# Kernel optimization log

Measured on AMD Instinct MI355X. Metric: run time of the kernel, lower is better.

## Reference

```python
import jax, jax.numpy as jnp
import numpy as np
import math

N_HEAD = 16
N_KV_HEAD = 4
HEAD_DIM = 128  # n_embed // n_head


def apply_rope(x, omega, offset=0):
    # x: (B, T, H, D); omega: (D//2,) Llama-style inverse frequencies
    T = x.shape[1]
    d2 = x.shape[-1] // 2
    pos = (jnp.arange(T) + offset).astype(x.dtype)
    ang = pos[:, None] * omega[None, :]              # (T, d2)
    cos = jnp.cos(ang)[None, :, None, :]
    sin = jnp.sin(ang)[None, :, None, :]
    x1, x2 = x[..., :d2], x[..., d2:]
    return jnp.concatenate([x1 * cos - x2 * sin, x1 * sin + x2 * cos], axis=-1)


def setup_inputs() -> dict:
    key = jax.random.key(0)
    k1, k2, k3, k4 = jax.random.split(key, 4)
    B, T, C = 2, 2048, 2048
    std = 0.02
    x = jax.random.normal(k1, (B, T, C), dtype=jnp.float32)
    wq = jax.random.normal(k2, (C, C), dtype=jnp.float32) * std
    wkv = jax.random.normal(k3, (C, 2 * N_KV_HEAD * HEAD_DIM), dtype=jnp.float32) * std
    wproj = jax.random.normal(k4, (C, C), dtype=jnp.float32) * std * (2 * 24) ** (-0.5)
    # Llama RoPE frequencies: 1 / 10000^(2i/D)
    omega = (1.0 / (10000.0 ** (jnp.arange(0, HEAD_DIM, 2, dtype=jnp.float32) / HEAD_DIM)))
    return {"x": x, "wq": wq, "wkv": wkv, "wproj": wproj, "omega": omega}


def reference(x, wq, wkv, wproj, omega):
    B, T, C = x.shape
    H, KH, D = N_HEAD, N_KV_HEAD, HEAD_DIM
    G = H // KH  # query heads per kv head

    q = (x @ wq).reshape(B, T, H, D)
    kv = x @ wkv
    k, v = jnp.split(kv, 2, axis=-1)

    q = apply_rope(q, omega, offset=0)
    k = apply_rope(k.reshape(B, T, KH, D), omega, offset=0)
    v = v.reshape(B, T, KH, D)

    # GQA causal attention (no KV expansion: group query heads per kv head)
    qr = q.reshape(B, T, KH, G, D)
    scores = jnp.einsum('bqkgd,bskd->bkgqs', qr, k) / math.sqrt(D)
    causal = jnp.tril(jnp.ones((T, T), dtype=bool))
    scores = jnp.where(causal[None, None, None, :, :], scores, -jnp.inf)
    att = jax.nn.softmax(scores, axis=-1)
    y = jnp.einsum('bkgqs,bskd->bqkgd', att, v).reshape(B, T, C)
    return y @ wproj
```

## Files before the change

kernel.cpp:

```cpp
#include <hip/hip_runtime.h>
#include <hip/hip_bf16.h>

#define B_ 2
#define T_ 2048
#define C_ 2048
#define H_ 16
#define KH_ 4
#define D_ 128

typedef unsigned short ushort_t;
typedef __attribute__((ext_vector_type(8))) short short8;
typedef __attribute__((ext_vector_type(4))) float f32x4;

#define RSQRT_D 0.08838834764831845f
#define L2E 1.4426950408889634f
#define QSCALE (0.08838834764831845f * 1.4426950408889634f)

__device__ __forceinline__ ushort_t f2b(float f) {
  union { float f; unsigned u; } v; v.f = f;
  unsigned r = v.u + 0x7fffu + ((v.u >> 16) & 1u);
  return (ushort_t)(r >> 16);
}
__device__ __forceinline__ float b2f(ushort_t u) {
  union { unsigned u; float f; } v; v.u = ((unsigned)u) << 16;
  return v.f;
}

__device__ __forceinline__ f32x4 mfma16(short8 a, short8 b, f32x4 c) {
  return __builtin_amdgcn_mfma_f32_16x16x32_bf16(a, b, c, 0, 0, 0);
}

__device__ __forceinline__ void async16(const void* g, void* l) {
  __builtin_amdgcn_global_load_lds(
      (const __attribute__((address_space(1))) void*)g,
      (__attribute__((address_space(3))) void*)l, 16, 0, 0);
}

__device__ __forceinline__ unsigned cvtpk(float lo, float hi) {
  unsigned r;
  asm volatile("v_cvt_pk_bf16_f32 %0, %1, %2" : "=v"(r) : "v"(lo), "v"(hi));
  return r;
}

__global__ __launch_bounds__(256) void prep_a(const float* __restrict__ x,
                                              const float* __restrict__ wq,
                                              const float* __restrict__ wkv,
                                              const float* __restrict__ wproj,
                                              const float* __restrict__ omega,
                                              ushort_t* __restrict__ xb,
                                              ushort_t* __restrict__ wqkvT,
                                              ushort_t* __restrict__ wprojT,
                                              float2* __restrict__ tab) {
  __shared__ float tile[32][33];
  int blk = blockIdx.x;
  const int tid = threadIdx.x;
  if (blk < 8192) {
    int i = blk * 256 + tid;
    float4 v = ((const float4*)x)[i];
    ushort4 o;
    o.x = f2b(v.x); o.y = f2b(v.y); o.z = f2b(v.z); o.w = f2b(v.w);
    ((ushort4*)xb)[i] = o;
    return;
  }
  blk -= 8192;
  if (blk < 10240) {
    const float* in;
    ushort_t* out;
    int Cc, gx, gy;
    if (blk < 4096)      { in = wq;    out = wqkvT;               Cc = 2048; gx = blk & 63;  gy = blk >> 6; }
    else if (blk < 6144) { int b2 = blk - 4096; in = wkv;  out = wqkvT + 2048 * 2048; Cc = 1024; gx = b2 & 31; gy = b2 >> 5; }
    else                 { int b2 = blk - 6144; in = wproj; out = wprojT;             Cc = 2048; gx = b2 & 63; gy = b2 >> 6; }
    const int c0 = gx * 32, r0 = gy * 32;
    const int tx = tid & 31, ty = tid >> 5;
#pragma unroll
    for (int i = 0; i < 4; i++) {
      int r = ty + i * 8;
      tile[r][tx] = in[(size_t)(r0 + r) * Cc + c0 + tx];
    }
    __syncthreads();
#pragma unroll
    for (int i = 0; i < 4; i++) {
      int r = ty + i * 8;
      out[(size_t)(c0 + r) * 2048 + r0 + tx] = f2b(tile[tx][r]);
    }
    return;
  }
  blk -= 10240;
  {
    int idx = blk * 256 + tid;
    int d = idx & 63;
    int t = idx >> 6;
    float ang = (float)t * omega[d];
    tab[idx] = make_float2(cosf(ang), sinf(ang));
  }
}

__global__ __launch_bounds__(256) void prep_b(const ushort_t* __restrict__ QKVraw,
                                              const float2* __restrict__ tab,
                                              ushort_t* __restrict__ Qb,
                                              ushort_t* __restrict__ Kb,
                                              ushort_t* __restrict__ Vf) {
  int blk = blockIdx.x;
  const int tid = threadIdx.x;
  if (blk < 4096) {
    int idx = blk * 256 + tid;
    int d4 = (idx & 15) * 4;
    int h = (idx >> 4) & 15;
    int t = (idx >> 8) & 2047;
    int b = idx >> 19;
    size_t in_off = (size_t)(b * 2048 + t) * 3072 + h * 128 + d4;
    ushort4 x1 = *(const ushort4*)(QKVraw + in_off);
    ushort4 x2 = *(const ushort4*)(QKVraw + in_off + 64);
    float4 csA = *(const float4*)(&tab[t * 64 + d4]);
    float4 csB = *(const float4*)(&tab[t * 64 + d4 + 2]);
    ushort4 o1, o2;
    o1.x = f2b((b2f(x1.x) * csA.x - b2f(x2.x) * csA.y) * QSCALE);
    o2.x = f2b((b2f(x1.x) * csA.y + b2f(x2.x) * csA.x) * QSCALE);
    o1.y = f2b((b2f(x1.y) * csA.z - b2f(x2.y) * csA.w) * QSCALE);
    o2.y = f2b((b2f(x1.y) * csA.w + b2f(x2.y) * csA.z) * QSCALE);
    o1.z = f2b((b2f(x1.z) * csB.x - b2f(x2.z) * csB.y) * QSCALE);
    o2.z = f2b((b2f(x1.z) * csB.y + b2f(x2.z) * csB.x) * QSCALE);
    o1.w = f2b((b2f(x1.w) * csB.z - b2f(x2.w) * csB.w) * QSCALE);
    o2.w = f2b((b2f(x1.w) * csB.w + b2f(x2.w) * csB.z) * QSCALE);
    size_t out_off = ((size_t)(b * 16 + h) * 2048 + t) * 128 + d4;
    *(ushort4*)(Qb + out_off) = o1;
    *(ushort4*)(Qb + out_off + 64) = o2;
    return;
  }
  if (blk < 5120) {
    int idx = (blk - 4096) * 256 + tid;
    int d4 = (idx & 15) * 4;
    int kh = (idx >> 4) & 3;
    int t = (idx >> 6) & 2047;
    int b = idx >> 17;
    size_t in_off = (size_t)(b * 2048 + t) * 3072 + 2048 + kh * 128 + d4;
    ushort4 x1 = *(const ushort4*)(QKVraw + in_off);
    ushort4 x2 = *(const ushort4*)(QKVraw + in_off + 64);
    float4 csA = *(const float4*)(&tab[t * 64 + d4]);
    float4 csB = *(const float4*)(&tab[t * 64 + d4 + 2]);
    ushort4 o1, o2;
    o1.x = f2b(b2f(x1.x) * csA.x - b2f(x2.x) * csA.y);
    o2.x = f2b(b2f(x1.x) * csA.y + b2f(x2.x) * csA.x);
    o1.y = f2b(b2f(x1.y) * csA.z - b2f(x2.y) * csA.w);
    o2.y = f2b(b2f(x1.y) * csA.w + b2f(x2.y) * csA.z);
    o1.z = f2b(b2f(x1.z) * csB.x - b2f(x2.z) * csB.y);
    o2.z = f2b(b2f(x1.z) * csB.y + b2f(x2.z) * csB.x);
    o1.w = f2b(b2f(x1.w) * csB.z - b2f(x2.w) * csB.w);
    o2.w = f2b(b2f(x1.w) * csB.w + b2f(x2.w) * csB.z);
    size_t out_off = ((size_t)(b * 4 + kh) * 2048 + t) * 128 + d4;
    *(ushort4*)(Kb + out_off) = o1;
    *(ushort4*)(Kb + out_off + 64) = o2;
    return;
  }
  {
    int idx = (blk - 5120) * 256 + tid;
    int lane = idx & 63;
    int n = (idx >> 6) & 7;
    int hv = (idx >> 9) & 1;
    int tile = (idx >> 10) & 31;
    int z = idx >> 15;
    int b = z >> 2, kh = z & 3;
    int lr = lane & 15, lc = lane >> 4;
    int d = n * 16 + lr;
    union { ushort_t u[8]; short8 v; } out;
#pragma unroll
    for (int j = 0; j < 8; j++) {
      int tw = j >> 1, par = j & 1;
      int kl = (hv * 2 + (tw >> 1)) * 16 + lc * 4 + 2 * (tw & 1) + par;
      int t = tile * 64 + kl;
      out.u[j] = QKVraw[(size_t)(b * 2048 + t) * 3072 + 2560 + kh * 128 + d];
    }
    *(short8*)(Vf + (size_t)idx * 8) = out.v;
  }
}

__device__ __forceinline__ void store_out(float* C, size_t idx, float v) { C[idx] = v; }
__device__ __forceinline__ void store_out(ushort_t* C, size_t idx, float v) { C[idx] = f2b(v); }


template <typename OUT_T>
__global__ __launch_bounds__(256) void gemm_bt(const ushort_t* __restrict__ A,
                                               const ushort_t* __restrict__ Bt,
                                               OUT_T* __restrict__ C,
                                               int M, int N, int K) {
  __shared__ __attribute__((aligned(16))) ushort_t As[2][128 * 32];
  __shared__ __attribute__((aligned(16))) ushort_t Bs[2][128 * 32];
  const int tid = threadIdx.x;
  const int lane = tid & 63;
  const int w = tid >> 6;
  const int bm = blockIdx.y, bn = blockIdx.x;
  const int lr = lane & 15, lc = lane >> 4;
  const int wr = (w >> 1) * 64, wc = (w & 1) * 64;
  const ushort_t* Ab = A + (size_t)bm * 128 * K;
  const ushort_t* Bb = Bt + (size_t)bn * 128 * K;
  const int srow = tid >> 2;
  const int scol = (tid & 3) * 8;
  f32x4 acc[4][4];
#pragma unroll
  for (int i = 0; i < 4; i++)
#pragma unroll
    for (int j = 0; j < 4; j++) acc[i][j] = (f32x4)(0.0f);

  async16(Ab + (size_t)srow * K + scol, &As[0][0] + srow * 32 + scol);
  async16(Ab + (size_t)(srow + 64) * K + scol, &As[0][0] + (srow + 64) * 32 + scol);
  async16(Bb + (size_t)srow * K + scol, &Bs[0][0] + srow * 32 + scol);
  async16(Bb + (size_t)(srow + 64) * K + scol, &Bs[0][0] + (srow + 64) * 32 + scol);

  const int nt = K >> 5;
#pragma unroll 2
  for (int t = 0; t < nt - 1; t++) {
    const int cur = t & 1;
    {
      const int k1 = (t + 1) << 5;
      ushort_t* Ad = &As[cur ^ 1][0];
      ushort_t* Bd = &Bs[cur ^ 1][0];
      async16(Ab + (size_t)srow * K + k1 + scol, Ad + srow * 32 + scol);
      async16(Ab + (size_t)(srow + 64) * K + k1 + scol, Ad + (srow + 64) * 32 + scol);
      async16(Bb + (size_t)srow * K + k1 + scol, Bd + srow * 32 + scol);
      async16(Bb + (size_t)(srow + 64) * K + k1 + scol, Bd + (srow + 64) * 32 + scol);
    }
    asm volatile("s_waitcnt vmcnt(4)" ::: "memory");
    __builtin_amdgcn_s_barrier();
    __builtin_amdgcn_sched_barrier(0);
    const ushort_t* Al = &As[cur][0];
    const ushort_t* Bl = &Bs[cur][0];
    short8 af[4], bf[4];
#pragma unroll
    for (int mi = 0; mi < 4; mi++)
      af[mi] = *(const short8*)(Al + (wr + mi * 16 + lr) * 32 + lc * 8);
#pragma unroll
    for (int ni = 0; ni < 4; ni++)
      bf[ni] = *(const short8*)(Bl + (wc + ni * 16 + lr) * 32 + lc * 8);
#pragma unroll
    for (int mi = 0; mi < 4; mi++)
#pragma unroll
      for (int ni = 0; ni < 4; ni++)
        acc[mi][ni] = mfma16(af[mi], bf[ni], acc[mi][ni]);
    asm volatile("" ::: "memory");
    __builtin_amdgcn_s_barrier();
    asm volatile("" ::: "memory");
  }
  {
    const int cur = (nt - 1) & 1;
    asm volatile("s_waitcnt vmcnt(0)" ::: "memory");
    __builtin_amdgcn_s_barrier();
    __builtin_amdgcn_sched_barrier(0);
    const ushort_t* Al = &As[cur][0];
    const ushort_t* Bl = &Bs[cur][0];
    short8 af[4], bf[4];
#pragma unroll
    for (int mi = 0; mi < 4; mi++)
      af[mi] = *(const short8*)(Al + (wr + mi * 16 + lr) * 32 + lc * 8);
#pragma unroll
    for (int ni = 0; ni < 4; ni++)
      bf[ni] = *(const short8*)(Bl + (wc + ni * 16 + lr) * 32 + lc * 8);
#pragma unroll
    for (int mi = 0; mi < 4; mi++)
#pragma unroll
      for (int ni = 0; ni < 4; ni++)
        acc[mi][ni] = mfma16(af[mi], bf[ni], acc[mi][ni]);
  }
#pragma unroll
  for (int mi = 0; mi < 4; mi++) {
#pragma unroll
    for (int ni = 0; ni < 4; ni++) {
      int row = bm * 128 + wr + mi * 16 + lc * 4;
      int col = bn * 128 + wc + ni * 16 + lr;
#pragma unroll
      for (int r = 0; r < 4; r++)
        store_out(C, (size_t)(row + r) * N + col, acc[mi][ni][r]);
    }
  }
}

__global__ __launch_bounds__(512, 1) void gemm256q(const ushort_t* __restrict__ A,
                                                   const ushort_t* __restrict__ Bt,
                                                   ushort_t* __restrict__ C,
                                                   int M, int N, int K) {
  __shared__ __attribute__((aligned(16))) ushort_t As[2][2][8192];
  __shared__ __attribute__((aligned(16))) ushort_t Bs[2][2][6144];
  __shared__ __attribute__((aligned(16))) ushort_t Scr[512];
  const int tid = threadIdx.x;
  const int lane = tid & 63;
  const int w = tid >> 6;
  const int lr = lane & 15, lc = lane >> 4;
  const int wm = w >> 2, wn = w & 3;
  const int nwg = gridDim.x;
  const int cpx = nwg >> 3;
  const int swz = (blockIdx.x & 7) * cpx + (blockIdx.x >> 3);
  const int bnc = N / 192;
  const int bm = swz / bnc, bn = swz % bnc;
  const ushort_t* Ab = A + (size_t)bm * 256 * K;
  const ushort_t* Bb = Bt + (size_t)bn * 192 * K;

  f32x4 acc[8][3];
#pragma unroll
  for (int i = 0; i < 8; i++)
#pragma unroll
    for (int j = 0; j < 3; j++) acc[i][j] = (f32x4)(0.0f);

  auto STAGE = [&](int kt, int hid) {
    const int buf = kt & 1;
    const int kk = hid >> 1;
    const int kbase = kt * 64 + kk * 32;
    if (!(hid & 1)) {
      ushort_t* db = &As[buf][kk][0];
      {
        const int u = tid, row = u >> 2, c = u & 3;
        const int lch = c ^ ((row >> 1) & 3);
        async16(Ab + (size_t)row * K + kbase + lch * 8, db + u * 8);
      }
      {
        const int u = 512 + tid, row = u >> 2, c = u & 3;
        const int lch = c ^ ((row >> 1) & 3);
        async16(Ab + (size_t)row * K + kbase + lch * 8, db + u * 8);
      }
    } else {
      ushort_t* db = &Bs[buf][kk][0];
      {
        const int u = tid, row = u >> 2, c = u & 3;
        const int lch = c ^ ((row >> 1) & 3);
        async16(Bb + (size_t)row * K + kbase + lch * 8, db + u * 8);
      }
      if (tid < 256) {
        const int u = 512 + tid, row = u >> 2, c = u & 3;
        const int lch = c ^ ((row >> 1) & 3);
        async16(Bb + (size_t)row * K + kbase + lch * 8, db + u * 8);
      } else {
        async16(Bb + (size_t)(tid & 255) * 8, &Scr[0]);
      }
    }
  };

  const int nt = K >> 6;
  STAGE(0, 0); STAGE(0, 1); STAGE(0, 2); STAGE(0, 3);
  asm volatile("s_waitcnt vmcnt(4)" ::: "memory");
  __builtin_amdgcn_s_barrier();

#pragma unroll 1
  for (int t = 0; t < nt; ++t) {
    const int buf = t & 1;
    const ushort_t* Ak0 = &As[buf][0][0];
    const ushort_t* Ak1 = &As[buf][1][0];
    const ushort_t* Bk0 = &Bs[buf][0][0];
    const ushort_t* Bk1 = &Bs[buf][1][0];
    short8 af[4], bf[3];

#pragma unroll
    for (int nf = 0; nf < 3; nf++) {
      const int row = wn * 48 + nf * 16 + lr;
      bf[nf] = *(const short8*)(Bk0 + row * 32 + ((lc ^ ((row >> 1) & 3)) * 8));
    }
#pragma unroll
    for (int mf = 0; mf < 4; mf++) {
      const int row = wm * 128 + mf * 16 + lr;
      af[mf] = *(const short8*)(Ak0 + row * 32 + ((lc ^ ((row >> 1) & 3)) * 8));
    }
    if (t + 1 < nt) STAGE(t + 1, 0);
    __builtin_amdgcn_s_barrier();
    asm volatile("s_waitcnt lgkmcnt(0)" ::: "memory");
    __builtin_amdgcn_sched_barrier(0);
    __builtin_amdgcn_s_setprio(1);
#pragma unroll
    for (int mf = 0; mf < 4; mf++)
#pragma unroll
      for (int nf = 0; nf < 3; nf++)
        acc[mf][nf] = mfma16(af[mf], bf[nf], acc[mf][nf]);
    __builtin_amdgcn_s_setprio(0);
    __builtin_amdgcn_s_barrier();

#pragma unroll
    for (int mf = 0; mf < 4; mf++) {
      const int row = wm * 128 + 64 + mf * 16 + lr;
      af[mf] = *(const short8*)(Ak0 + row * 32 + ((lc ^ ((row >> 1) & 3)) * 8));
    }
    if (t + 1 < nt) STAGE(t + 1, 1);
    __builtin_amdgcn_s_barrier();
    asm volatile("s_waitcnt lgkmcnt(0)" ::: "memory");
    __builtin_amdgcn_sched_barrier(0);
    __builtin_amdgcn_s_setprio(1);
#pragma unroll
    for (int mf = 0; mf < 4; mf++)
#pragma unroll
      for (int nf = 0; nf < 3; nf++)
        acc[4 + mf][nf] = mfma16(af[mf], bf[nf], acc[4 + mf][nf]);
    __builtin_amdgcn_s_setprio(0);
    if (t + 1 < nt) {
      asm volatile("s_waitcnt vmcnt(4)" ::: "memory");
    } else {
      asm volatile("s_waitcnt vmcnt(0)" ::: "memory");
    }
    __builtin_amdgcn_s_barrier();

#pragma unroll
    for (int nf = 0; nf < 3; nf++) {
      const int row = wn * 48 + nf * 16 + lr;
      bf[nf] = *(const short8*)(Bk1 + row * 32 + ((lc ^ ((row >> 1) & 3)) * 8));
    }
#pragma unroll
    for (int mf = 0; mf < 4; mf++) {
      const int row = wm * 128 + mf * 16 + lr;
      af[mf] = *(const short8*)(Ak1 + row * 32 + ((lc ^ ((row >> 1) & 3)) * 8));
    }
    if (t + 1 < nt) STAGE(t + 1, 2);
    __builtin_amdgcn_s_barrier();
    asm volatile("s_waitcnt lgkmcnt(0)" ::: "memory");
    __builtin_amdgcn_sched_barrier(0);
    __builtin_amdgcn_s_setprio(1);
#pragma unroll
    for (int mf = 0; mf < 4; mf++)
#pragma unroll
      for (int nf = 0; nf < 3; nf++)
        acc[mf][nf] = mfma16(af[mf], bf[nf], acc[mf][nf]);
    __builtin_amdgcn_s_setprio(0);
    __builtin_amdgcn_s_barrier();

#pragma unroll
    for (int mf = 0; mf < 4; mf++) {
      const int row = wm * 128 + 64 + mf * 16 + lr;
      af[mf] = *(const short8*)(Ak1 + row * 32 + ((lc ^ ((row >> 1) & 3)) * 8));
    }
    if (t + 1 < nt) STAGE(t + 1, 3);
    __builtin_amdgcn_s_barrier();
    asm volatile("s_waitcnt lgkmcnt(0)" ::: "memory");
    __builtin_amdgcn_sched_barrier(0);
    __builtin_amdgcn_s_setprio(1);
#pragma unroll
    for (int mf = 0; mf < 4; mf++)
#pragma unroll
      for (int nf = 0; nf < 3; nf++)
        acc[4 + mf][nf] = mfma16(af[mf], bf[nf], acc[4 + mf][nf]);
    __builtin_amdgcn_s_setprio(0);
    if (t + 1 < nt) {
      asm volatile("s_waitcnt vmcnt(4)" ::: "memory");
    }
    __builtin_amdgcn_s_barrier();
  }

#pragma unroll
  for (int mfp = 0; mfp < 8; mfp++) {
#pragma unroll
    for (int nf = 0; nf < 3; nf++) {
      const int row = bm * 256 + wm * 128 + mfp * 16 + lc * 4;
      const int col = bn * 192 + wn * 48 + nf * 16 + lr;
#pragma unroll
      for (int r = 0; r < 4; r++)
        C[(size_t)(row + r) * N + col] = f2b(acc[mfp][nf][r]);
    }
  }
}

__global__ __launch_bounds__(256, 2) void attn_k(const ushort_t* __restrict__ Qb,
                                                 const ushort_t* __restrict__ Kb,
                                                 const ushort_t* __restrict__ Vf,
                                                 ushort_t* __restrict__ Yb) {
  __shared__ __attribute__((aligned(16))) ushort_t Ks[2][64 * 128];
  const int tid = threadIdx.x;
  const int lane = tid & 63;
  const int w = tid >> 6;
  const int lr = lane & 15, lc = lane >> 4;
  const int gy = blockIdx.y;
  const int h = gy;
  const int b = blockIdx.z;
  const int kh = h >> 2;
  const int qc = b ? (15 - ((blockIdx.x + gy) & 15)) : ((blockIdx.x + gy) & 15);
  const int q0w = qc * 128 + w * 32;

  const ushort_t* Qp = Qb + (size_t)(b * 16 + h) * T_ * D_;
  const ushort_t* Kp = Kb + (size_t)(b * 4 + kh) * T_ * D_;
  const ushort_t* Vfb = Vf + (size_t)(b * 4 + kh) * 262144;

  const int st_row = tid >> 4;
  const int st_slot = tid & 15;

  short8 qf[2][4];
#pragma unroll
  for (int f = 0; f < 2; f++)
#pragma unroll
    for (int c = 0; c < 4; c++)
      qf[f][c] = *(const short8*)(Qp + (size_t)(q0w + f * 16 + lr) * D_ + c * 32 + lc * 8);

  f32x4 o[2][8];
#pragma unroll
  for (int f = 0; f < 2; f++)
#pragma unroll
    for (int n = 0; n < 8; n++) o[f][n] = (f32x4)(0.0f);
  float m[2] = {-1e30f, -1e30f}, l[2] = {0.0f, 0.0f};

  const int nt = 2 * qc + 2;

#pragma unroll
  for (int i = 0; i < 4; i++) {
    int row = i * 16 + st_row;
    async16(Kp + (size_t)row * D_ + (((st_slot - row) & 15) * 8),
            &Ks[0][0] + row * 128 + st_slot * 8);
  }

#pragma unroll 1
  for (int ti = 0; ti < nt; ti++) {
    __syncthreads();
    const int kv0 = ti * 64;
    if (ti + 1 < nt) {
      const ushort_t* Kn = Kp + (size_t)(kv0 + 64) * D_;
      ushort_t* dst = &Ks[(ti + 1) & 1][0];
#pragma unroll
      for (int i = 0; i < 4; i++) {
        int row = i * 16 + st_row;
        async16(Kn + (size_t)row * D_ + (((st_slot - row) & 15) * 8),
                dst + row * 128 + st_slot * 8);
      }
    }
    if (kv0 > q0w + 31) continue;
    const ushort_t* Kl = &Ks[ti & 1][0];
    const ushort_t* Vt0 = Vfb + (size_t)(ti * 2) * 4096;
    short8 vr0[8];
#pragma unroll
    for (int n = 0; n < 8; n++)
      vr0[n] = *(const short8*)(Vt0 + n * 512 + lane * 8);
    f32x4 s[2][4];
#pragma unroll
    for (int f = 0; f < 2; f++)
#pragma unroll
      for (int kj = 0; kj < 4; kj++) s[f][kj] = (f32x4)(0.0f);
    __builtin_amdgcn_s_setprio(1);
#pragma unroll
    for (int c = 0; c < 4; c++) {
      short8 kf[4];
#pragma unroll
      for (int kj = 0; kj < 4; kj++)
        kf[kj] = *(const short8*)(Kl + (kj * 16 + lr) * 128 + (((c * 4 + lc + lr) & 15) * 8));
#pragma unroll
      for (int f = 0; f < 2; f++)
#pragma unroll
        for (int kj = 0; kj < 4; kj++)
          s[f][kj] = mfma16(kf[kj], qf[f][c], s[f][kj]);
    }
    __builtin_amdgcn_s_setprio(0);
    const ushort_t* Vt1 = Vfb + (size_t)(ti * 2 + 1) * 4096;
    short8 vr1[8];
#pragma unroll
    for (int n = 0; n < 8; n++)
      vr1[n] = *(const short8*)(Vt1 + n * 512 + lane * 8);
    const bool maskt = (kv0 + 63 > q0w);
    union { unsigned u[4]; short8 v; } pa0[2], pa1[2];
#pragma unroll
    for (int f = 0; f < 2; f++) {
      const int q = q0w + f * 16 + lr;
      float pv[16];
      float mx = -1e30f;
      if (maskt) {
#pragma unroll
        for (int kj = 0; kj < 4; kj++)
#pragma unroll
          for (int r = 0; r < 4; r++) {
            float a = s[f][kj][r];
            if (kv0 + kj * 16 + lc * 4 + r > q) a = -1e30f;
            pv[kj * 4 + r] = a;
            mx = fmaxf(mx, a);
          }
      } else {
#pragma unroll
        for (int kj = 0; kj < 4; kj++)
#pragma unroll
          for (int r = 0; r < 4; r++) {
            float a = s[f][kj][r];
            pv[kj * 4 + r] = a;
            mx = fmaxf(mx, a);
          }
      }
      mx = fmaxf(mx, __shfl_xor(mx, 16));
      mx = fmaxf(mx, __shfl_xor(mx, 32));
      const bool need = __any(mx > m[f] + 8.0f);
      const float mn = need ? fmaxf(m[f], mx) : m[f];
      float rs = 0.0f;
#pragma unroll
      for (int i = 0; i < 16; i++) {
        pv[i] = exp2f(pv[i] - mn);
        rs += pv[i];
      }
      rs += __shfl_xor(rs, 16);
      rs += __shfl_xor(rs, 32);
#pragma unroll
      for (int kj = 0; kj < 2; kj++) {
        pa0[f].u[kj * 2] = cvtpk(pv[kj * 4], pv[kj * 4 + 1]);
        pa0[f].u[kj * 2 + 1] = cvtpk(pv[kj * 4 + 2], pv[kj * 4 + 3]);
        pa1[f].u[kj * 2] = cvtpk(pv[8 + kj * 4], pv[8 + kj * 4 + 1]);
        pa1[f].u[kj * 2 + 1] = cvtpk(pv[8 + kj * 4 + 2], pv[8 + kj * 4 + 3]);
      }
      if (need) {
        float al = exp2f(m[f] - mn);
        m[f] = mn;
        l[f] = l[f] * al + rs;
        float alT[4];
#pragma unroll
        for (int r = 0; r < 4; r++)
          alT[r] = __shfl(al, (lane & 48) | (lc * 4 + r));
#pragma unroll
        for (int n = 0; n < 8; n++)
#pragma unroll
          for (int r = 0; r < 4; r++) o[f][n][r] *= alT[r];
      } else {
        l[f] += rs;
      }
    }
    __builtin_amdgcn_s_setprio(1);
#pragma unroll
    for (int n = 0; n < 8; n++) {
      o[0][n] = mfma16(pa0[0].v, vr0[n], o[0][n]);
      o[1][n] = mfma16(pa0[1].v, vr0[n], o[1][n]);
    }
#pragma unroll
    for (int n = 0; n < 8; n++) {
      o[0][n] = mfma16(pa1[0].v, vr1[n], o[0][n]);
      o[1][n] = mfma16(pa1[1].v, vr1[n], o[1][n]);
    }
    __builtin_amdgcn_s_setprio(0);
  }
#pragma unroll
  for (int f = 0; f < 2; f++) {
    float inv = 1.0f / l[f];
    float invT[4];
#pragma unroll
    for (int r = 0; r < 4; r++)
      invT[r] = __shfl(inv, (lane & 48) | (lc * 4 + r));
#pragma unroll
    for (int n = 0; n < 8; n++)
#pragma unroll
      for (int r = 0; r < 4; r++) {
        int qo = q0w + f * 16 + lc * 4 + r;
        int d = n * 16 + lr;
        Yb[(size_t)(b * T_ + qo) * 2048 + h * 128 + d] = f2b(o[f][n][r] * invT[r]);
      }
  }
}


extern "C" void kernel_launch(void* const* d_in, const int* in_sizes, int n_in,
                              void* d_out, int out_size, void* d_ws, size_t ws_size,
                              hipStream_t stream) {
  (void)in_sizes; (void)n_in; (void)out_size; (void)ws_size;
  const float* x = (const float*)d_in[0];
  const float* wq = (const float*)d_in[1];
  const float* wkv = (const float*)d_in[2];
  const float* wproj = (const float*)d_in[3];
  const float* omega = (const float*)d_in[4];
  float* out = (float*)d_out;
  char* ws = (char*)d_ws;

  ushort_t* xb     = (ushort_t*)(ws + 0);
  ushort_t* wqkvT  = (ushort_t*)(ws + 16777216);
  ushort_t* wprojT = (ushort_t*)(ws + 29360128);
  ushort_t* QKVraw = (ushort_t*)(ws + 37748736);
  ushort_t* Qb     = (ushort_t*)(ws + 62914560);
  ushort_t* Kb     = (ushort_t*)(ws + 79691776);
  ushort_t* Vf     = (ushort_t*)(ws + 83886080);
  ushort_t* Yb     = (ushort_t*)(ws + 88080384);
  float2*   tab    = (float2*)(ws + 104857600);

  prep_a<<<18944, 256, 0, stream>>>(x, wq, wkv, wproj, omega, xb, wqkvT, wprojT, tab);

  gemm256q<<<256, 512, 0, stream>>>(xb, wqkvT, QKVraw, 4096, 3072, 2048);

  prep_b<<<6144, 256, 0, stream>>>(QKVraw, tab, Qb, Kb, Vf);

  attn_k<<<dim3(16, 16, 2), 256, 0, stream>>>(Qb, Kb, Vf, Yb);

  gemm_bt<<<dim3(16, 32), 256, 0, stream>>>(Yb, wprojT, out, 4096, 2048, 2048);
}
```

Baseline: 206.3 us.

## Replace projection GEMM with 128x256 tile, 512-thread swizzled kernel

The output projection GEMM moves from a 128x128 tile with 256 threads to a 128x256 tile with 8 waves and 512 threads. It uses a 64-deep K pipeline with double buffering, an XOR-swizzled LDS layout to avoid bank conflicts, and a block-index swizzle for L2 locality. It also raises wave priority around the MFMA bursts. The aim is better reuse per block and less LDS conflict overhead. The cost is a grid of only 256 workgroups at one block per CU, which may leave some CUs idle.

```diff
diff --git a/kernel.cpp b/kernel.cpp
--- a/kernel.cpp
+++ b/kernel.cpp
@@ -147,7 +147,7 @@
     o2.z = f2b(b2f(x1.z) * csB.y + b2f(x2.z) * csB.x);
     o1.w = f2b(b2f(x1.w) * csB.z - b2f(x2.w) * csB.w);
     o2.w = f2b(b2f(x1.w) * csB.w + b2f(x2.w) * csB.z);
-    size_t out_off = ((size_t)(b * 4 + kh) * 2048 + t) * 128 + d4;
+    size_t out_off = (size_t)(b * 4 + kh) * 2048 * 128 + (size_t)t * 128 + d4;
     *(ushort4*)(Kb + out_off) = o1;
     *(ushort4*)(Kb + out_off + 64) = o2;
     return;
@@ -174,101 +174,107 @@
   }
 }
 
-__device__ __forceinline__ void store_out(float* C, size_t idx, float v) { C[idx] = v; }
-__device__ __forceinline__ void store_out(ushort_t* C, size_t idx, float v) { C[idx] = f2b(v); }
-
-
-template <typename OUT_T>
-__global__ __launch_bounds__(256) void gemm_bt(const ushort_t* __restrict__ A,
-                                               const ushort_t* __restrict__ Bt,
-                                               OUT_T* __restrict__ C,
-                                               int M, int N, int K) {
-  __shared__ __attribute__((aligned(16))) ushort_t As[2][128 * 32];
-  __shared__ __attribute__((aligned(16))) ushort_t Bs[2][128 * 32];
+__global__ __launch_bounds__(512, 1) void gemm_proj(const ushort_t* __restrict__ A,
+                                                    const ushort_t* __restrict__ Bt,
+                                                    float* __restrict__ C,
+                                                    int M, int N, int K) {
+  __shared__ __attribute__((aligned(16))) ushort_t As[2][2][4096];
+  __shared__ __attribute__((aligned(16))) ushort_t Bs[2][2][8192];
   const int tid = threadIdx.x;
   const int lane = tid & 63;
   const int w = tid >> 6;
-  const int bm = blockIdx.y, bn = blockIdx.x;
   const int lr = lane & 15, lc = lane >> 4;
-  const int wr = (w >> 1) * 64, wc = (w & 1) * 64;
+  const int wm = w >> 2, wn = w & 3;
+  const int nwg = gridDim.x;
+  const int cpx = nwg >> 3;
+  const int swz = (blockIdx.x & 7) * cpx + (blockIdx.x >> 3);
+  const int bnc = N >> 8;
+  const int bm = swz / bnc, bn = swz % bnc;
   const ushort_t* Ab = A + (size_t)bm * 128 * K;
-  const ushort_t* Bb = Bt + (size_t)bn * 128 * K;
-  const int srow = tid >> 2;
-  const int scol = (tid & 3) * 8;
+  const ushort_t* Bb = Bt + (size_t)bn * 256 * K;
+
   f32x4 acc[4][4];
 #pragma unroll
   for (int i = 0; i < 4; i++)
 #pragma unroll
     for (int j = 0; j < 4; j++) acc[i][j] = (f32x4)(0.0f);
 
-  async16(Ab + (size_t)srow * K + scol, &As[0][0] + srow * 32 + scol);
-  async16(Ab + (size_t)(srow + 64) * K + scol, &As[0][0] + (srow + 64) * 32 + scol);
-  async16(Bb + (size_t)srow * K + scol, &Bs[0][0] + srow * 32 + scol);
-  async16(Bb + (size_t)(srow + 64) * K + scol, &Bs[0][0] + (srow + 64) * 32 + scol);
-
-  const int nt = K >> 5;
-#pragma unroll 2
-  for (int t = 0; t < nt - 1; t++) {
-    const int cur = t & 1;
+  auto STAGE = [&](int kt, int kk) {
+    const int buf = kt & 1;
+    const int kbase = kt * 64 + kk * 32;
     {
-      const int k1 = (t + 1) << 5;
-      ushort_t* Ad = &As[cur ^ 1][0];
-      ushort_t* Bd = &Bs[cur ^ 1][0];
-      async16(Ab + (size_t)srow * K + k1 + scol, Ad + srow * 32 + scol);
-      async16(Ab + (size_t)(srow + 64) * K + k1 + scol, Ad + (srow + 64) * 32 + scol);
-      async16(Bb + (size_t)srow * K + k1 + scol, Bd + srow * 32 + scol);
-      async16(Bb + (size_t)(srow + 64) * K + k1 + scol, Bd + (srow + 64) * 32 + scol);
-    }
-    asm volatile("s_waitcnt vmcnt(4)" ::: "memory");
-    __builtin_amdgcn_s_barrier();
-    __builtin_amdgcn_sched_barrier(0);
-    const ushort_t* Al = &As[cur][0];
-    const ushort_t* Bl = &Bs[cur][0];
-    short8 af[4], bf[4];
-#pragma unroll
-    for (int mi = 0; mi < 4; mi++)
-      af[mi] = *(const short8*)(Al + (wr + mi * 16 + lr) * 32 + lc * 8);
-#pragma unroll
-    for (int ni = 0; ni < 4; ni++)
-      bf[ni] = *(const short8*)(Bl + (wc + ni * 16 + lr) * 32 + lc * 8);
-#pragma unroll
-    for (int mi = 0; mi < 4; mi++)
-#pragma unroll
-      for (int ni = 0; ni < 4; ni++)
-        acc[mi][ni] = mfma16(af[mi], bf[ni], acc[mi][ni]);
-    asm volatile("" ::: "memory");
-    __builtin_amdgcn_s_barrier();
-    asm volatile("" ::: "memory");
-  }
-  {
-    const int cur = (nt - 1) & 1;
-    asm volatile("s_waitcnt vmcnt(0)" ::: "memory");
-    __builtin_amdgcn_s_barrier();
-    __builtin_amdgcn_sched_barrier(0);
-    const ushort_t* Al = &As[cur][0];
-    const ushort_t* Bl = &Bs[cur][0];
-    short8 af[4], bf[4];
-#pragma unroll
-    for (int mi = 0; mi < 4; mi++)
-      af[mi] = *(const short8*)(Al + (wr + mi * 16 + lr) * 32 + lc * 8);
-#pragma unroll
-    for (int ni = 0; ni < 4; ni++)
-      bf[ni] = *(const short8*)(Bl + (wc + ni * 16 + lr) * 32 + lc * 8);
-#pragma unroll
-    for (int mi = 0; mi < 4; mi++)
-#pragma unroll
-      for (int ni = 0; ni < 4; ni++)
-        acc[mi][ni] = mfma16(af[mi], bf[ni], acc[mi][ni]);
-  }
-#pragma unroll
-  for (int mi = 0; mi < 4; mi++) {
-#pragma unroll
-    for (int ni = 0; ni < 4; ni++) {
-      int row = bm * 128 + wr + mi * 16 + lc * 4;
-      int col = bn * 128 + wc + ni * 16 + lr;
+      ushort_t* db = &As[buf][kk][0];
+      const int u = tid, row = u >> 2, c = u & 3;
+      const int lch = c ^ ((row >> 1) & 3);
+      async16(Ab + (size_t)row * K + kbase + lch * 8, db + u * 8);
+    }
+    {
+      ushort_t* db = &Bs[buf][kk][0];
+      {
+        const int u = tid, row = u >> 2, c = u & 3;
+        const int lch = c ^ ((row >> 1) & 3);
+        async16(Bb + (size_t)row * K + kbase + lch * 8, db + u * 8);
+      }
+      {
+        const int u = 512 + tid, row = u >> 2, c = u & 3;
+        const int lch = c ^ ((row >> 1) & 3);
+        async16(Bb + (size_t)row * K + kbase + lch * 8, db + u * 8);
+      }
+    }
+  };
+
+  const int nt = K >> 6;
+  STAGE(0, 0); STAGE(0, 1);
+  asm volatile("s_waitcnt vmcnt(3)" ::: "memory");
+  __builtin_amdgcn_s_barrier();
+
+#pragma unroll 1
+  for (int t = 0; t < nt; ++t) {
+    const int buf = t & 1;
+#pragma unroll
+    for (int kk = 0; kk < 2; kk++) {
+      const ushort_t* Ak = &As[buf][kk][0];
+      const ushort_t* Bk = &Bs[buf][kk][0];
+      short8 af[4], bf[4];
+#pragma unroll
+      for (int mf = 0; mf < 4; mf++) {
+        const int row = wm * 64 + mf * 16 + lr;
+        af[mf] = *(const short8*)(Ak + row * 32 + ((lc ^ ((row >> 1) & 3)) * 8));
+      }
+#pragma unroll
+      for (int nf = 0; nf < 4; nf++) {
+        const int row = wn * 64 + nf * 16 + lr;
+        bf[nf] = *(const short8*)(Bk + row * 32 + ((lc ^ ((row >> 1) & 3)) * 8));
+      }
+      if (t + 1 < nt) STAGE(t + 1, kk);
+      __builtin_amdgcn_s_barrier();
+      asm volatile("s_waitcnt lgkmcnt(0)" ::: "memory");
+      __builtin_amdgcn_sched_barrier(0);
+      __builtin_amdgcn_s_setprio(1);
+#pragma unroll
+      for (int mf = 0; mf < 4; mf++)
+#pragma unroll
+        for (int nf = 0; nf < 4; nf++)
+          acc[mf][nf] = mfma16(af[mf], bf[nf], acc[mf][nf]);
+      __builtin_amdgcn_s_setprio(0);
+      if (t + 1 < nt) {
+        asm volatile("s_waitcnt vmcnt(3)" ::: "memory");
+      } else if (kk == 0) {
+        asm volatile("s_waitcnt vmcnt(0)" ::: "memory");
+      }
+      __builtin_amdgcn_s_barrier();
+    }
+  }
+
+#pragma unroll
+  for (int mf = 0; mf < 4; mf++) {
+#pragma unroll
+    for (int nf = 0; nf < 4; nf++) {
+      const int row = bm * 128 + wm * 64 + mf * 16 + lc * 4;
+      const int col = bn * 256 + wn * 64 + nf * 16 + lr;
 #pragma unroll
       for (int r = 0; r < 4; r++)
-        store_out(C, (size_t)(row + r) * N + col, acc[mi][ni][r]);
+        C[(size_t)(row + r) * N + col] = acc[mf][nf][r];
     }
   }
 }
@@ -665,5 +671,5 @@
 
   attn_k<<<dim3(16, 16, 2), 256, 0, stream>>>(Qb, Kb, Vf, Yb);
 
-  gemm_bt<<<dim3(16, 32), 256, 0, stream>>>(Yb, wprojT, out, 4096, 2048, 2048);
-}
+  gemm_proj<<<256, 512, 0, stream>>>(Yb, wprojT, out, 4096, 2048, 2048);
+}
```

Result: no change. 204.2 us (median of 2 runs) (-1.0%).
